# Optimization experiments

Measured on AMD Instinct MI355X. Metric: run time of the kernel, lower is better.

Reference implementation:

```python
import jax, jax.numpy as jnp
import numpy as np


def setup_inputs() -> dict:
    key = jax.random.key(0)
    ks = jax.random.split(key, 6)
    B, N1, N2 = 4, 16384, 4096
    C1, C2 = 128, 256
    H1, H2 = 256, 128
    Cin = C1 + C2  # 384
    return {
        "xyz1": jax.random.normal(ks[0], (B, N1, 3), dtype=jnp.float32),
        "xyz2": jax.random.normal(ks[1], (B, N2, 3), dtype=jnp.float32),
        "features1": jax.random.normal(ks[2], (B, N1, C1), dtype=jnp.float32),
        "features2": jax.random.normal(ks[3], (B, N2, C2), dtype=jnp.float32),
        "W1": jax.random.normal(ks[4], (Cin, H1), dtype=jnp.float32) * (1.0 / np.sqrt(Cin)),
        "b1": jnp.zeros((H1,), dtype=jnp.float32),
        "W2": jax.random.normal(ks[5], (H1, H2), dtype=jnp.float32) * (1.0 / np.sqrt(H1)),
        "b2": jnp.zeros((H2,), dtype=jnp.float32),
    }


def reference(xyz1, xyz2, features1, features2, W1, b1, W2, b2):
    # Pairwise squared distances: [B, N1, N2]
    diff = xyz1[:, :, None, :] - xyz2[:, None, :, :]
    dist = jnp.sum(diff * diff, axis=-1)
    # 3 smallest distances (tf.argsort ascending, take first 3)
    neg_d3, idx = jax.lax.top_k(-dist, 3)          # idx: [B, N1, 3]
    d3 = jnp.maximum(-neg_d3, 1e-10)
    w = 1.0 / d3
    w = w / jnp.sum(w, axis=-1, keepdims=True)      # [B, N1, 3]
    # Gather features2 at the 3-NN indices per batch: [B, N1, 3, C2]
    gathered = jax.vmap(lambda f, i: f[i])(features2, idx)
    interp = jnp.sum(gathered * w[..., None], axis=2)  # [B, N1, C2]
    new_features = jnp.concatenate([interp, features1], axis=-1)  # [B, N1, C1+C2]
    # Pointwise MLP (Dense + ReLU, no BN)
    h = jax.nn.relu(jnp.einsum("bnc,ch->bnh", new_features, W1) + b1)
    out = jax.nn.relu(jnp.einsum("bnh,ho->bno", h, W2) + b2)
    return out
```

## Files before the change

### kernel.cpp

```cpp
#include <hip/hip_runtime.h>
#include <hip/hip_bf16.h>

typedef __bf16 bf16_t;
typedef __attribute__((ext_vector_type(8))) __bf16 bf16x8;
typedef __attribute__((ext_vector_type(4))) __bf16 bf16x4;
typedef __attribute__((ext_vector_type(4))) float f32x4;

#define N1 16384
#define N2 4096
#define C1 128
#define C2 256
#define CIN 384
#define HD1 256
#define HD2 128
#define BDIM 4
#define CHUNK 512
#define NCHUNK 8
#define NCAND 24

__global__ void prep_w(const float* __restrict__ W1, const float* __restrict__ W2,
                       bf16_t* __restrict__ W1t, bf16_t* __restrict__ W2t) {
  int tid = blockIdx.x * 256 + threadIdx.x;
  if (tid < CIN * HD1) {
    int k = tid / HD1, n = tid % HD1;
    W1t[n * CIN + k] = (bf16_t)W1[tid];
  }
  if (tid < HD1 * HD2) {
    int k = tid / HD2, n = tid % HD2;
    W2t[n * HD1 + k] = (bf16_t)W2[tid];
  }
}

__global__ __launch_bounds__(256) void knn_chunk(
    const float* __restrict__ xyz1, const float* __restrict__ xyz2,
    float* __restrict__ candd, int* __restrict__ candj) {
  int b  = blockIdx.y;
  int ck = blockIdx.z;
  int i  = blockIdx.x * 256 + threadIdx.x;
  const float* p = xyz1 + ((size_t)b * N1 + i) * 3;
  float px = p[0], py = p[1], pz = p[2];

  const float* x2b = xyz2 + ((size_t)b * N2 + (size_t)ck * CHUNK) * 3;

  float d0 = 3.4e38f, d1 = 3.4e38f, d2 = 3.4e38f;
  int   j0 = 0, j1 = 0, j2 = 0;

  for (int j = 0; j < CHUNK; j += 16) {
    float c[48];
    const float4* q = (const float4*)(x2b + 3 * j);
#pragma unroll
    for (int t = 0; t < 12; ++t) {
      float4 v = q[t];
      c[4 * t + 0] = v.x; c[4 * t + 1] = v.y; c[4 * t + 2] = v.z; c[4 * t + 3] = v.w;
    }
#pragma unroll
    for (int u = 0; u < 16; ++u) {
      float dx = __fsub_rn(c[3 * u + 0], px);
      float dy = __fsub_rn(c[3 * u + 1], py);
      float dz = __fsub_rn(c[3 * u + 2], pz);
      float d = __fadd_rn(__fadd_rn(__fmul_rn(dx, dx), __fmul_rn(dy, dy)),
                          __fmul_rn(dz, dz));
      int jj = j + u;
      if (d < d2) {
        bool lt0 = d < d0, lt1 = d < d1;
        j2 = lt1 ? j1 : jj;
        j1 = lt0 ? j0 : (lt1 ? jj : j1);
        j0 = lt0 ? jj : j0;
        d2 = __builtin_amdgcn_fmed3f(d, d1, d2);
        d1 = __builtin_amdgcn_fmed3f(d, d0, d1);
        d0 = fminf(d, d0);
      }
    }
  }
  size_t qb = ((size_t)b * N1 + i) * NCAND + (size_t)ck * 3;
  int jbase = ck * CHUNK;
  candd[qb + 0] = d0; candd[qb + 1] = d1; candd[qb + 2] = d2;
  candj[qb + 0] = j0 + jbase; candj[qb + 1] = j1 + jbase; candj[qb + 2] = j2 + jbase;
}

__global__ __launch_bounds__(256) void knn_merge(
    const float* __restrict__ candd, const int* __restrict__ candj,
    float* __restrict__ wq, int* __restrict__ iq) {
  int q = blockIdx.x * 256 + threadIdx.x;
  const float* cd = candd + (size_t)q * NCAND;
  const int*   cj = candj + (size_t)q * NCAND;
  float d0 = 3.4e38f, d1 = 3.4e38f, d2 = 3.4e38f;
  int   j0 = 0, j1 = 0, j2 = 0;
#pragma unroll
  for (int c = 0; c < NCAND; ++c) {
    float d = cd[c]; int j = cj[c];
    bool p0 = d < d0, p1 = d < d1, p2 = d < d2;
    j2 = p1 ? j1 : (p2 ? j : j2);
    j1 = p0 ? j0 : (p1 ? j : j1);
    j0 = p0 ? j : j0;
    d2 = __builtin_amdgcn_fmed3f(d, d1, d2);
    d1 = __builtin_amdgcn_fmed3f(d, d0, d1);
    d0 = fminf(d, d0);
  }
  d0 = fmaxf(d0, 1e-10f); d1 = fmaxf(d1, 1e-10f); d2 = fmaxf(d2, 1e-10f);
  float w0 = 1.0f / d0, w1 = 1.0f / d1, w2 = 1.0f / d2;
  float ws = w0 + w1 + w2;
  wq[q * 3 + 0] = w0 / ws; wq[q * 3 + 1] = w1 / ws; wq[q * 3 + 2] = w2 / ws;
  iq[q * 3 + 0] = j0; iq[q * 3 + 1] = j1; iq[q * 3 + 2] = j2;
}

__global__ __launch_bounds__(256) void interp_concat(
    const float* __restrict__ f1, const float* __restrict__ f2,
    const float* __restrict__ wq, const int* __restrict__ iq,
    bf16_t* __restrict__ NF) {
  int wv = threadIdx.x >> 6, ln = threadIdx.x & 63;
  size_t q = (size_t)blockIdx.x * 4 + wv;
  int b = (int)(q >> 14);
  float u0 = wq[q * 3 + 0], u1 = wq[q * 3 + 1], u2 = wq[q * 3 + 2];
  const float* f2b = f2 + (size_t)b * N2 * C2;
  const float* r0 = f2b + (size_t)iq[q * 3 + 0] * C2;
  const float* r1 = f2b + (size_t)iq[q * 3 + 1] * C2;
  const float* r2 = f2b + (size_t)iq[q * 3 + 2] * C2;
  int c = ln * 4;
  float4 v0 = *(const float4*)(r0 + c);
  float4 v1 = *(const float4*)(r1 + c);
  float4 v2 = *(const float4*)(r2 + c);
  bf16x4 o;
  o[0] = (bf16_t)(u0 * v0.x + u1 * v1.x + u2 * v2.x);
  o[1] = (bf16_t)(u0 * v0.y + u1 * v1.y + u2 * v2.y);
  o[2] = (bf16_t)(u0 * v0.z + u1 * v1.z + u2 * v2.z);
  o[3] = (bf16_t)(u0 * v0.w + u1 * v1.w + u2 * v2.w);
  *(bf16x4*)(NF + q * CIN + c) = o;
  if (ln < 32) {
    float4 g = *(const float4*)(f1 + q * C1 + c);
    bf16x4 og;
    og[0] = (bf16_t)g.x; og[1] = (bf16_t)g.y; og[2] = (bf16_t)g.z; og[3] = (bf16_t)g.w;
    *(bf16x4*)(NF + q * CIN + C2 + c) = og;
  }
}

template <bool OUT_BF16>
__global__ __launch_bounds__(256) void gemm_bt(
    const bf16_t* __restrict__ A, const bf16_t* __restrict__ Bt,
    const float* __restrict__ bias, void* __restrict__ Cout,
    int M, int N, int K) {
  __shared__ __align__(16) bf16_t As[128 * 32];
  __shared__ __align__(16) bf16_t Bs[128 * 32];
  int tid  = threadIdx.x;
  int wv   = tid >> 6, ln = tid & 63;
  int quad = ln >> 4, lm = ln & 15;
  long row0 = (long)blockIdx.x * 128;
  int  col0 = blockIdx.y * 128;
  const bf16_t* Ab = A + row0 * K;
  const bf16_t* Bb = Bt + (long)col0 * K;
  f32x4 acc[4][4] = {};
  int wm = (wv >> 1) * 64, wn = (wv & 1) * 64;

  for (int k0 = 0; k0 < K; k0 += 32) {
#pragma unroll
    for (int t = 0; t < 2; ++t) {
      int c = t * 256 + tid;
      int r = c >> 2, kc = (c & 3) << 3;
      __builtin_amdgcn_global_load_lds(
          (const __attribute__((address_space(1))) void*)(Ab + (long)r * K + k0 + kc),
          (__attribute__((address_space(3))) void*)(As + (t * 256 + wv * 64) * 8),
          16, 0, 0);
      __builtin_amdgcn_global_load_lds(
          (const __attribute__((address_space(1))) void*)(Bb + (long)r * K + k0 + kc),
          (__attribute__((address_space(3))) void*)(Bs + (t * 256 + wv * 64) * 8),
          16, 0, 0);
    }
    __syncthreads();
    bf16x8 af[4], bfr[4];
#pragma unroll
    for (int mi = 0; mi < 4; ++mi)
      af[mi] = *(const bf16x8*)(As + (wm + mi * 16 + lm) * 32 + quad * 8);
#pragma unroll
    for (int ni = 0; ni < 4; ++ni)
      bfr[ni] = *(const bf16x8*)(Bs + (wn + ni * 16 + lm) * 32 + quad * 8);
#pragma unroll
    for (int mi = 0; mi < 4; ++mi)
#pragma unroll
      for (int ni = 0; ni < 4; ++ni)
        acc[mi][ni] = __builtin_amdgcn_mfma_f32_16x16x32_bf16(af[mi], bfr[ni],
                                                              acc[mi][ni], 0, 0, 0);
    __syncthreads();
  }

#pragma unroll
  for (int mi = 0; mi < 4; ++mi)
#pragma unroll
    for (int ni = 0; ni < 4; ++ni) {
      int col = col0 + wn + ni * 16 + lm;
      float bv = bias[col];
#pragma unroll
      for (int r = 0; r < 4; ++r) {
        long rowg = row0 + wm + mi * 16 + quad * 4 + r;
        float v = acc[mi][ni][r] + bv;
        v = fmaxf(v, 0.0f);
        if (OUT_BF16) ((bf16_t*)Cout)[rowg * N + col] = (bf16_t)v;
        else          ((float*)Cout)[rowg * N + col]  = v;
      }
    }
}

extern "C" void kernel_launch(void* const* d_in, const int* in_sizes, int n_in,
                              void* d_out, int out_size, void* d_ws, size_t ws_size,
                              hipStream_t stream) {
  const float* xyz1 = (const float*)d_in[0];
  const float* xyz2 = (const float*)d_in[1];
  const float* f1   = (const float*)d_in[2];
  const float* f2   = (const float*)d_in[3];
  const float* W1   = (const float*)d_in[4];
  const float* b1   = (const float*)d_in[5];
  const float* W2   = (const float*)d_in[6];
  const float* b2   = (const float*)d_in[7];
  float* out = (float*)d_out;

  const size_t NQ = (size_t)BDIM * N1;
  char* ws = (char*)d_ws;
  bf16_t* W1t = (bf16_t*)ws;
  bf16_t* W2t = (bf16_t*)(ws + (256 << 10));
  float*  wq  = (float*)(ws + (512 << 10));
  int*    iq  = (int*)(ws + (1536 << 10));
  bf16_t* NF  = (bf16_t*)(ws + (2560 << 10));
  char*   hb  = ws + (2560 << 10) + NQ * CIN * 2;
  bf16_t* Hbuf  = (bf16_t*)hb;
  float*  candd = (float*)hb;
  int*    candj = (int*)(hb + NQ * NCAND * 4);

  prep_w<<<dim3(384), dim3(256), 0, stream>>>(W1, W2, W1t, W2t);
  knn_chunk<<<dim3(N1 / 256, BDIM, NCHUNK), dim3(256), 0, stream>>>(
      xyz1, xyz2, candd, candj);
  knn_merge<<<dim3(NQ / 256), dim3(256), 0, stream>>>(candd, candj, wq, iq);
  interp_concat<<<dim3(NQ / 4), dim3(256), 0, stream>>>(f1, f2, wq, iq, NF);
  gemm_bt<true><<<dim3(NQ / 128, HD1 / 128), dim3(256), 0, stream>>>(
      NF, W1t, b1, (void*)Hbuf, NQ, HD1, CIN);
  gemm_bt<false><<<dim3(NQ / 128, HD2 / 128), dim3(256), 0, stream>>>(
      Hbuf, W2t, b2, (void*)out, NQ, HD2, HD1);
}
```

Before: 264.2 us.

## Fuse interpolation and concat into first MLP GEMM producer stage

Replaces the separate interp_concat kernel and first GEMM with one kernel. Each block builds its 128-row A tile on the fly by gathering the three neighbour feature rows, weighting them, or converting features1 to bf16, and writes the tile straight to LDS. Each block also covers all 256 output columns, so A is built once per row. This removes the bf16 NF buffer round trip through global memory and one launch. In exchange the gather loads sit in the GEMM main loop without double buffering, and the larger accumulator raises register pressure.

```diff
diff --git a/kernel.cpp b/kernel.cpp
--- a/kernel.cpp
+++ b/kernel.cpp
@@ -104,34 +104,107 @@
   iq[q * 3 + 0] = j0; iq[q * 3 + 1] = j1; iq[q * 3 + 2] = j2;
 }
 
-__global__ __launch_bounds__(256) void interp_concat(
+__global__ __launch_bounds__(256, 2) void interp_gemm1(
     const float* __restrict__ f1, const float* __restrict__ f2,
     const float* __restrict__ wq, const int* __restrict__ iq,
-    bf16_t* __restrict__ NF) {
-  int wv = threadIdx.x >> 6, ln = threadIdx.x & 63;
-  size_t q = (size_t)blockIdx.x * 4 + wv;
-  int b = (int)(q >> 14);
+    const bf16_t* __restrict__ W1t, const float* __restrict__ b1,
+    bf16_t* __restrict__ Hbuf) {
+  __shared__ __align__(16) bf16_t As[128 * 32];
+  __shared__ __align__(16) bf16_t Bs[4 * 256 * 8];
+  int tid  = threadIdx.x;
+  int wv   = tid >> 6, ln = tid & 63;
+  int quad = ln >> 4, lm = ln & 15;
+  long row0 = (long)blockIdx.x * 128;
+
+  int srow = tid >> 1;
+  int sh   = tid & 1;
+  long q = row0 + srow;
+  int  b = (int)(q >> 14);
   float u0 = wq[q * 3 + 0], u1 = wq[q * 3 + 1], u2 = wq[q * 3 + 2];
   const float* f2b = f2 + (size_t)b * N2 * C2;
   const float* r0 = f2b + (size_t)iq[q * 3 + 0] * C2;
   const float* r1 = f2b + (size_t)iq[q * 3 + 1] * C2;
   const float* r2 = f2b + (size_t)iq[q * 3 + 2] * C2;
-  int c = ln * 4;
-  float4 v0 = *(const float4*)(r0 + c);
-  float4 v1 = *(const float4*)(r1 + c);
-  float4 v2 = *(const float4*)(r2 + c);
-  bf16x4 o;
-  o[0] = (bf16_t)(u0 * v0.x + u1 * v1.x + u2 * v2.x);
-  o[1] = (bf16_t)(u0 * v0.y + u1 * v1.y + u2 * v2.y);
-  o[2] = (bf16_t)(u0 * v0.z + u1 * v1.z + u2 * v2.z);
-  o[3] = (bf16_t)(u0 * v0.w + u1 * v1.w + u2 * v2.w);
-  *(bf16x4*)(NF + q * CIN + c) = o;
-  if (ln < 32) {
-    float4 g = *(const float4*)(f1 + q * C1 + c);
-    bf16x4 og;
-    og[0] = (bf16_t)g.x; og[1] = (bf16_t)g.y; og[2] = (bf16_t)g.z; og[3] = (bf16_t)g.w;
-    *(bf16x4*)(NF + q * CIN + C2 + c) = og;
-  }
+  const float* f1r = f1 + (size_t)q * C1;
+  bf16_t* asd = As + srow * 32 + sh * 16;
+
+  int wm = (wv >> 1) * 64, wn = (wv & 1) * 128;
+  f32x4 acc[4][8] = {};
+
+  for (int ks = 0; ks < 12; ++ks) {
+    int kb = ks * 32;
+#pragma unroll
+    for (int s = 0; s < 4; ++s) {
+      __builtin_amdgcn_global_load_lds(
+          (const __attribute__((address_space(1))) void*)(
+              W1t + (size_t)(wv * 64 + ln) * CIN + kb + s * 8),
+          (__attribute__((address_space(3))) void*)(Bs + s * 2048 + wv * 512),
+          16, 0, 0);
+    }
+    bf16x8 o[2];
+    if (ks < 8) {
+      int cb = kb + sh * 16;
+#pragma unroll
+      for (int c4 = 0; c4 < 4; ++c4) {
+        float4 v0 = *(const float4*)(r0 + cb + c4 * 4);
+        float4 v1 = *(const float4*)(r1 + cb + c4 * 4);
+        float4 v2 = *(const float4*)(r2 + cb + c4 * 4);
+        int oi = c4 >> 1, off = (c4 & 1) * 4;
+        o[oi][off + 0] = (bf16_t)(u0 * v0.x + u1 * v1.x + u2 * v2.x);
+        o[oi][off + 1] = (bf16_t)(u0 * v0.y + u1 * v1.y + u2 * v2.y);
+        o[oi][off + 2] = (bf16_t)(u0 * v0.z + u1 * v1.z + u2 * v2.z);
+        o[oi][off + 3] = (bf16_t)(u0 * v0.w + u1 * v1.w + u2 * v2.w);
+      }
+    } else {
+      int cf = kb - 256 + sh * 16;
+#pragma unroll
+      for (int c4 = 0; c4 < 4; ++c4) {
+        float4 g = *(const float4*)(f1r + cf + c4 * 4);
+        int oi = c4 >> 1, off = (c4 & 1) * 4;
+        o[oi][off + 0] = (bf16_t)g.x;
+        o[oi][off + 1] = (bf16_t)g.y;
+        o[oi][off + 2] = (bf16_t)g.z;
+        o[oi][off + 3] = (bf16_t)g.w;
+      }
+    }
+    *(bf16x8*)(asd) = o[0];
+    *(bf16x8*)(asd + 8) = o[1];
+    __syncthreads();
+
+    bf16x8 af[4];
+#pragma unroll
+    for (int mi = 0; mi < 4; ++mi)
+      af[mi] = *(const bf16x8*)(As + (wm + mi * 16 + lm) * 32 + quad * 8);
+#pragma unroll
+    for (int nh = 0; nh < 2; ++nh) {
+      bf16x8 bfr[4];
+#pragma unroll
+      for (int nn = 0; nn < 4; ++nn)
+        bfr[nn] = *(const bf16x8*)(Bs + quad * 2048 + (wn + (nh * 4 + nn) * 16 + lm) * 8);
+#pragma unroll
+      for (int mi = 0; mi < 4; ++mi)
+#pragma unroll
+        for (int nn = 0; nn < 4; ++nn)
+          acc[mi][nh * 4 + nn] = __builtin_amdgcn_mfma_f32_16x16x32_bf16(
+              af[mi], bfr[nn], acc[mi][nh * 4 + nn], 0, 0, 0);
+    }
+    __syncthreads();
+  }
+
+#pragma unroll
+  for (int mi = 0; mi < 4; ++mi)
+#pragma unroll
+    for (int ni = 0; ni < 8; ++ni) {
+      int col = wn + ni * 16 + lm;
+      float bv = b1[col];
+#pragma unroll
+      for (int r = 0; r < 4; ++r) {
+        long rowg = row0 + wm + mi * 16 + quad * 4 + r;
+        float v = acc[mi][ni][r] + bv;
+        v = fmaxf(v, 0.0f);
+        Hbuf[rowg * HD1 + col] = (bf16_t)v;
+      }
+    }
 }
 
 template <bool OUT_BF16>
@@ -218,7 +291,6 @@
   bf16_t* W2t = (bf16_t*)(ws + (256 << 10));
   float*  wq  = (float*)(ws + (512 << 10));
   int*    iq  = (int*)(ws + (1536 << 10));
-  bf16_t* NF  = (bf16_t*)(ws + (2560 << 10));
   char*   hb  = ws + (2560 << 10) + NQ * CIN * 2;
   bf16_t* Hbuf  = (bf16_t*)hb;
   float*  candd = (float*)hb;
@@ -228,9 +300,8 @@
   knn_chunk<<<dim3(N1 / 256, BDIM, NCHUNK), dim3(256), 0, stream>>>(
       xyz1, xyz2, candd, candj);
   knn_merge<<<dim3(NQ / 256), dim3(256), 0, stream>>>(candd, candj, wq, iq);
-  interp_concat<<<dim3(NQ / 4), dim3(256), 0, stream>>>(f1, f2, wq, iq, NF);
-  gemm_bt<true><<<dim3(NQ / 128, HD1 / 128), dim3(256), 0, stream>>>(
-      NF, W1t, b1, (void*)Hbuf, NQ, HD1, CIN);
+  interp_gemm1<<<dim3(NQ / 128), dim3(256), 0, stream>>>(
+      f1, f2, wq, iq, W1t, b1, Hbuf);
   gemm_bt<false><<<dim3(NQ / 128, HD2 / 128), dim3(256), 0, stream>>>(
       Hbuf, W2t, b2, (void*)out, NQ, HD2, HD1);
 }
```

New measurement: 256.4 us. 1.03x faster.
